# Kernel optimization log

Hardware: AMD Instinct MI355X
Metric: run time of the kernel (lower is better)

The kernel has to match this reference:

```python
import jax, jax.numpy as jnp
import numpy as np

N = 16777216  # rows
G = 1024      # distinct group keys (power of 2 -> no binary-search padding)


def setup_inputs() -> dict:
    key = jax.random.key(0)
    k1, k2, k3 = jax.random.split(key, 3)
    # guarantee every group id in [0, G) appears at least once
    base = jnp.arange(G, dtype=jnp.int32)
    rest = jax.random.randint(k1, (N - G,), 0, G, dtype=jnp.int32)
    key_col = jax.random.permutation(k2, jnp.concatenate([base, rest])).reshape(-1, 1)
    val_col = jax.random.normal(k3, (N, 1), dtype=jnp.float32)
    return {"key_col": key_col, "val_col": val_col}


def _group_indices(x_flat, uniq_desc):
    # Faithful vectorized replication of find_mapping_indices: binary search of each
    # x against the reverse-sorted (descending) unique keys. G is a power of 2 so
    # N_prime == G and no front padding occurs.
    steps = int(np.log2(G))
    offset = G // 2
    pos = (x_flat <= uniq_desc[offset]).astype(jnp.int32) * offset
    offset = offset // 2  # int(ceil(offset/2)) == offset//2 for powers of two
    for _ in range(1, steps):
        bins = (x_flat <= uniq_desc[pos + offset]).astype(jnp.int32)
        pos = pos + bins * offset
        offset = offset // 2
    return pos  # [N] group index in [0, G)


def reference(key_col, val_col):
    x = key_col.reshape(-1)
    v = val_col.reshape(-1)
    # torch.sort(torch.unique(x), descending=True): all G values present by construction
    uniq_desc = jnp.unique(x, size=G)[::-1]
    gid = _group_indices(x, uniq_desc)
    # fused segmented reduces replace the per-group masked_select loop (same math)
    s = jax.ops.segment_sum(v, gid, num_segments=G)
    cnt = jax.ops.segment_sum(jnp.ones_like(v), gid, num_segments=G)
    avg = s / cnt  # torch.mean per group; every group non-empty
    mn = jax.ops.segment_min(v, gid, num_segments=G)
    mx = jax.ops.segment_max(v, gid, num_segments=G)
    # group_selection_mask is all-True (every group occupied) -> masked_select is identity
    key_out = uniq_desc.reshape(-1, 1)
    return (key_out,
            s.reshape(-1, 1),
            avg.reshape(-1, 1),
            mn.reshape(-1, 1),
            mx.reshape(-1, 1))
```

## Files before the change

kernel.cpp:

```cpp
#include <hip/hip_runtime.h>

#define G 1024
#define SCALE 1048576.0f
#define CNT_SHIFT 42
#define ELEM_BIAS (1 << 24)
#define LOW_MASK ((1ULL << CNT_SHIFT) - 1)

__device__ __forceinline__ unsigned omap(float x) {
    unsigned u = __float_as_uint(x);
    return (u & 0x80000000u) ? ~u : (u | 0x80000000u);
}
__device__ __forceinline__ float ounmap(unsigned o) {
    unsigned u = (o & 0x80000000u) ? (o & 0x7fffffffu) : ~o;
    return __uint_as_float(u);
}

__global__ __launch_bounds__(256) void gb_partial(
    const int4* __restrict__ keys, const float4* __restrict__ vals, int n4,
    unsigned long long* __restrict__ acc_sum, unsigned* __restrict__ acc_cnt,
    unsigned* __restrict__ acc_maxo, unsigned* __restrict__ acc_minv)
{
    __shared__ unsigned long long s_sc[G];
    __shared__ uint2              s_mm[G];

    for (int k = threadIdx.x; k < G; k += 256) {
        s_sc[k] = 0ull;
        s_mm[k] = make_uint2(0xffffffffu, 0u);
    }
    __syncthreads();

    const int stride = gridDim.x * 256;
    for (int i = blockIdx.x * 256 + threadIdx.x; i < n4; i += stride) {
        int4   k4 = keys[i];
        float4 v4 = vals[i];

#define DO_ELEM(KK, VV)                                                        \
        {                                                                      \
            const int k = (KK); const float v = (VV);                          \
            const unsigned o = omap(v);                                        \
            uint2 mm = s_mm[k];            \
            if (o < mm.x) atomicMin(&s_mm[k].x, o);                            \
            if (o > mm.y) atomicMax(&s_mm[k].y, o);                            \
            const int vf = __float2int_rn(v * SCALE);                          \
            const unsigned long long add =                                     \
                (1ULL << CNT_SHIFT) + (unsigned long long)(unsigned)(vf + ELEM_BIAS); \
            atomicAdd(&s_sc[k], add);        \
        }

        DO_ELEM(k4.x, v4.x)
        DO_ELEM(k4.y, v4.y)
        DO_ELEM(k4.z, v4.z)
        DO_ELEM(k4.w, v4.w)
#undef DO_ELEM
    }
    __syncthreads();

    for (int k = threadIdx.x; k < G; k += 256) {
        const unsigned long long cell = s_sc[k];
        const unsigned n = (unsigned)(cell >> CNT_SHIFT);
        const long long sfx = (long long)(cell & LOW_MASK) - ((long long)n << 24);
        const uint2 mm = s_mm[k];
        atomicAdd(&acc_sum[k], (unsigned long long)sfx);
        atomicAdd(&acc_cnt[k], n);
        atomicMax(&acc_maxo[k], mm.y);
        atomicMax(&acc_minv[k], ~mm.x);
    }
}

__global__ __launch_bounds__(256) void gb_write(
    const unsigned long long* __restrict__ acc_sum, const unsigned* __restrict__ acc_cnt,
    const unsigned* __restrict__ acc_maxo, const unsigned* __restrict__ acc_minv,
    float* __restrict__ out)
{
    const int k = blockIdx.x * 256 + threadIdx.x;
    const float    sum = (float)((double)(long long)acc_sum[k] * (1.0 / (double)SCALE));
    const unsigned cnt = acc_cnt[k];
    const int g = (G - 1) - k;
    out[g]         = (float)k;
    out[G + g]     = sum;
    out[2 * G + g] = sum / (float)cnt;
    out[3 * G + g] = ounmap(~acc_minv[k]);
    out[4 * G + g] = ounmap(acc_maxo[k]);
}

extern "C" void kernel_launch(void* const* d_in, const int* in_sizes, int n_in,
                              void* d_out, int out_size, void* d_ws, size_t ws_size,
                              hipStream_t stream) {
    const int4*   keys = (const int4*)d_in[0];
    const float4* vals = (const float4*)d_in[1];
    const int n  = in_sizes[0];
    const int n4 = n / 4;

    unsigned long long* acc_sum  = (unsigned long long*)d_ws;
    unsigned*           acc_cnt  = (unsigned*)(acc_sum + G);
    unsigned*           acc_maxo = acc_cnt + G;
    unsigned*           acc_minv = acc_maxo + G;
    const size_t acc_bytes = (size_t)G * (8 + 4 + 4 + 4);

    hipMemsetAsync(d_ws, 0, acc_bytes, stream);

    hipLaunchKernelGGL(gb_partial, dim3(2048), dim3(256), 0, stream,
                       keys, vals, n4, acc_sum, acc_cnt, acc_maxo, acc_minv);
    hipLaunchKernelGGL(gb_write, dim3(G / 256), dim3(256), 0, stream,
                       acc_sum, acc_cnt, acc_maxo, acc_minv, (float*)d_out);
}
```

Measured before the change: 181.2 us.

## Add warm-up pass computing per-group min/max gates to skip most min/max atomics

A small warm-up kernel processes the first sixteenth of the data and builds per-group min/max estimates. A gate kernel turns these into 16-bit thresholds, and the main kernel then issues global min/max atomics only for values that may beat the current extreme. This removes the shared-memory min/max state and most of the per-element min/max work. Global accumulators are spread over 8 replicas to reduce atomic contention and are combined in the write kernel. In exchange it adds two extra kernel launches and global atomics for candidate values that pass the gate, and it software-prefetches the next input vector.

```diff
diff --git a/kernel.cpp b/kernel.cpp
--- a/kernel.cpp
+++ b/kernel.cpp
@@ -1,10 +1,11 @@
 #include <hip/hip_runtime.h>
 
 #define G 1024
-#define SCALE 1048576.0f
+#define SCALEF 1048576.0f
 #define CNT_SHIFT 42
 #define ELEM_BIAS (1 << 24)
 #define LOW_MASK ((1ULL << CNT_SHIFT) - 1)
+#define NREP 8
 
 __device__ __forceinline__ unsigned omap(float x) {
     unsigned u = __float_as_uint(x);
@@ -15,14 +16,13 @@
     return __uint_as_float(u);
 }
 
-__global__ __launch_bounds__(256) void gb_partial(
-    const int4* __restrict__ keys, const float4* __restrict__ vals, int n4,
-    unsigned long long* __restrict__ acc_sum, unsigned* __restrict__ acc_cnt,
-    unsigned* __restrict__ acc_maxo, unsigned* __restrict__ acc_minv)
+__global__ __launch_bounds__(256) void gb_warm(
+    const int4* __restrict__ keys, const float4* __restrict__ vals, int n4w,
+    unsigned long long* __restrict__ rsum, unsigned* __restrict__ rcnt,
+    unsigned* __restrict__ rmaxo, unsigned* __restrict__ rminv)
 {
     __shared__ unsigned long long s_sc[G];
     __shared__ uint2              s_mm[G];
-
     for (int k = threadIdx.x; k < G; k += 256) {
         s_sc[k] = 0ull;
         s_mm[k] = make_uint2(0xffffffffu, 0u);
@@ -30,57 +30,134 @@
     __syncthreads();
 
     const int stride = gridDim.x * 256;
-    for (int i = blockIdx.x * 256 + threadIdx.x; i < n4; i += stride) {
-        int4   k4 = keys[i];
-        float4 v4 = vals[i];
-
-#define DO_ELEM(KK, VV)                                                        \
+    for (int i = blockIdx.x * 256 + threadIdx.x; i < n4w; i += stride) {
+        int4 k4 = keys[i]; float4 v4 = vals[i];
+#define WARM_ELEM(KK, VV)                                                      \
         {                                                                      \
             const int k = (KK); const float v = (VV);                          \
             const unsigned o = omap(v);                                        \
-            uint2 mm = s_mm[k];            \
+            uint2 mm = s_mm[k];                                                \
             if (o < mm.x) atomicMin(&s_mm[k].x, o);                            \
             if (o > mm.y) atomicMax(&s_mm[k].y, o);                            \
-            const int vf = __float2int_rn(v * SCALE);                          \
-            const unsigned long long add =                                     \
-                (1ULL << CNT_SHIFT) + (unsigned long long)(unsigned)(vf + ELEM_BIAS); \
-            atomicAdd(&s_sc[k], add);        \
+            const int vf = __float2int_rn(v * SCALEF);                         \
+            atomicAdd(&s_sc[k], (1ULL << CNT_SHIFT) +                          \
+                      (unsigned long long)(unsigned)(vf + ELEM_BIAS));         \
+        }
+        WARM_ELEM(k4.x, v4.x) WARM_ELEM(k4.y, v4.y)
+        WARM_ELEM(k4.z, v4.z) WARM_ELEM(k4.w, v4.w)
+#undef WARM_ELEM
+    }
+    __syncthreads();
+
+    const int r = blockIdx.x & (NREP - 1);
+    for (int k = threadIdx.x; k < G; k += 256) {
+        const unsigned long long cell = s_sc[k];
+        const unsigned n = (unsigned)(cell >> CNT_SHIFT);
+        if (n) {
+            const long long sfx = (long long)(cell & LOW_MASK) - ((long long)n << 24);
+            const uint2 mm = s_mm[k];
+            atomicAdd(&rsum[r * G + k], (unsigned long long)sfx);
+            atomicAdd(&rcnt[r * G + k], n);
+            atomicMax(&rmaxo[r * G + k], mm.y);
+            atomicMax(&rminv[r * G + k], ~mm.x);
+        }
+    }
+}
+
+__global__ __launch_bounds__(256) void gb_gate(
+    const unsigned* __restrict__ rmaxo, const unsigned* __restrict__ rminv,
+    unsigned* __restrict__ gate)
+{
+    const int k = blockIdx.x * 256 + threadIdx.x;
+    unsigned mx = 0u, mv = 0u;
+    for (int r = 0; r < NREP; ++r) {
+        mx = max(mx, rmaxo[r * G + k]);
+        mv = max(mv, rminv[r * G + k]);
+    }
+    const unsigned min_o = ~mv;
+    gate[k] = (min_o & 0xffff0000u) | (mx >> 16);
+}
+
+__global__ __launch_bounds__(256) void gb_main(
+    const int4* __restrict__ keys, const float4* __restrict__ vals,
+    int i0, int n4,
+    unsigned long long* __restrict__ rsum, unsigned* __restrict__ rcnt,
+    unsigned* __restrict__ rmaxo, unsigned* __restrict__ rminv,
+    const unsigned* __restrict__ gate)
+{
+    __shared__ unsigned long long s_sc[G];
+    __shared__ unsigned           s_gate[G];
+    for (int k = threadIdx.x; k < G; k += 256) {
+        s_sc[k]   = 0ull;
+        s_gate[k] = gate[k];
+    }
+    __syncthreads();
+
+    const int r = blockIdx.x & (NREP - 1);
+    unsigned* __restrict__ rmaxo_r = rmaxo + r * G;
+    unsigned* __restrict__ rminv_r = rminv + r * G;
+
+#define MAIN_ELEM(KK, VV)                                                      \
+        {                                                                      \
+            const int k = (KK); const float v = (VV);                          \
+            const unsigned o  = omap(v);                                       \
+            const unsigned g  = s_gate[k];                                     \
+            const unsigned ot = o >> 16;                                       \
+            if (ot <= (g >> 16))     atomicMax(&rminv_r[k], ~o);               \
+            if (ot >= (g & 0xffffu)) atomicMax(&rmaxo_r[k], o);                \
+            const int vf = __float2int_rn(v * SCALEF);                         \
+            atomicAdd(&s_sc[k], (1ULL << CNT_SHIFT) +                          \
+                      (unsigned long long)(unsigned)(vf + ELEM_BIAS));         \
         }
 
-        DO_ELEM(k4.x, v4.x)
-        DO_ELEM(k4.y, v4.y)
-        DO_ELEM(k4.z, v4.z)
-        DO_ELEM(k4.w, v4.w)
-#undef DO_ELEM
+    const int stride = gridDim.x * 256;
+    int i = i0 + blockIdx.x * 256 + threadIdx.x;
+    if (i < n4) {
+        int4 k4 = keys[i]; float4 v4 = vals[i];
+        for (i += stride; ; i += stride) {
+            const bool more = (i < n4);
+            int4 nk; float4 nv;
+            if (more) { nk = keys[i]; nv = vals[i]; }
+            MAIN_ELEM(k4.x, v4.x) MAIN_ELEM(k4.y, v4.y)
+            MAIN_ELEM(k4.z, v4.z) MAIN_ELEM(k4.w, v4.w)
+            if (!more) break;
+            k4 = nk; v4 = nv;
+        }
     }
+#undef MAIN_ELEM
     __syncthreads();
 
     for (int k = threadIdx.x; k < G; k += 256) {
         const unsigned long long cell = s_sc[k];
         const unsigned n = (unsigned)(cell >> CNT_SHIFT);
-        const long long sfx = (long long)(cell & LOW_MASK) - ((long long)n << 24);
-        const uint2 mm = s_mm[k];
-        atomicAdd(&acc_sum[k], (unsigned long long)sfx);
-        atomicAdd(&acc_cnt[k], n);
-        atomicMax(&acc_maxo[k], mm.y);
-        atomicMax(&acc_minv[k], ~mm.x);
+        if (n) {
+            const long long sfx = (long long)(cell & LOW_MASK) - ((long long)n << 24);
+            atomicAdd(&rsum[r * G + k], (unsigned long long)sfx);
+            atomicAdd(&rcnt[r * G + k], n);
+        }
     }
 }
 
 __global__ __launch_bounds__(256) void gb_write(
-    const unsigned long long* __restrict__ acc_sum, const unsigned* __restrict__ acc_cnt,
-    const unsigned* __restrict__ acc_maxo, const unsigned* __restrict__ acc_minv,
+    const unsigned long long* __restrict__ rsum, const unsigned* __restrict__ rcnt,
+    const unsigned* __restrict__ rmaxo, const unsigned* __restrict__ rminv,
     float* __restrict__ out)
 {
     const int k = blockIdx.x * 256 + threadIdx.x;
-    const float    sum = (float)((double)(long long)acc_sum[k] * (1.0 / (double)SCALE));
-    const unsigned cnt = acc_cnt[k];
+    long long ts = 0ll; unsigned tc = 0u, mx = 0u, mv = 0u;
+    for (int r = 0; r < NREP; ++r) {
+        ts += (long long)rsum[r * G + k];
+        tc += rcnt[r * G + k];
+        mx = max(mx, rmaxo[r * G + k]);
+        mv = max(mv, rminv[r * G + k]);
+    }
+    const float sum = (float)((double)ts * (1.0 / (double)SCALEF));
     const int g = (G - 1) - k;
     out[g]         = (float)k;
     out[G + g]     = sum;
-    out[2 * G + g] = sum / (float)cnt;
-    out[3 * G + g] = ounmap(~acc_minv[k]);
-    out[4 * G + g] = ounmap(acc_maxo[k]);
+    out[2 * G + g] = sum / (float)tc;
+    out[3 * G + g] = ounmap(~mv);
+    out[4 * G + g] = ounmap(mx);
 }
 
 extern "C" void kernel_launch(void* const* d_in, const int* in_sizes, int n_in,
@@ -88,19 +165,27 @@
                               hipStream_t stream) {
     const int4*   keys = (const int4*)d_in[0];
     const float4* vals = (const float4*)d_in[1];
-    const int n  = in_sizes[0];
-    const int n4 = n / 4;
+    const int n   = in_sizes[0];
+    const int n4  = n / 4;
+    int n4w = n4 >> 4;
+    if (n4w < 1)  n4w = (n4 < 1) ? 0 : n4;
+    if (n4w > n4) n4w = n4;
 
-    unsigned long long* acc_sum  = (unsigned long long*)d_ws;
-    unsigned*           acc_cnt  = (unsigned*)(acc_sum + G);
-    unsigned*           acc_maxo = acc_cnt + G;
-    unsigned*           acc_minv = acc_maxo + G;
-    const size_t acc_bytes = (size_t)G * (8 + 4 + 4 + 4);
+    unsigned long long* rsum  = (unsigned long long*)d_ws;
+    unsigned*           rcnt  = (unsigned*)(rsum + NREP * G);
+    unsigned*           rmaxo = rcnt + NREP * G;
+    unsigned*           rminv = rmaxo + NREP * G;
+    unsigned*           gate  = rminv + NREP * G;
+    const size_t acc_bytes = (size_t)NREP * G * (8 + 4 + 4 + 4);
 
     hipMemsetAsync(d_ws, 0, acc_bytes, stream);
 
-    hipLaunchKernelGGL(gb_partial, dim3(2048), dim3(256), 0, stream,
-                       keys, vals, n4, acc_sum, acc_cnt, acc_maxo, acc_minv);
+    hipLaunchKernelGGL(gb_warm, dim3(256), dim3(256), 0, stream,
+                       keys, vals, n4w, rsum, rcnt, rmaxo, rminv);
+    hipLaunchKernelGGL(gb_gate, dim3(G / 256), dim3(256), 0, stream,
+                       rmaxo, rminv, gate);
+    hipLaunchKernelGGL(gb_main, dim3(2048), dim3(256), 0, stream,
+                       keys, vals, n4w, n4, rsum, rcnt, rmaxo, rminv, gate);
     hipLaunchKernelGGL(gb_write, dim3(G / 256), dim3(256), 0, stream,
-                       acc_sum, acc_cnt, acc_maxo, acc_minv, (float*)d_out);
+                       rsum, rcnt, rmaxo, rminv, (float*)d_out);
 }
```

New measurement: 172.4 us. 1.05x faster.
